# Kernel optimization log

Hardware: AMD Instinct MI355X
Metric: run time of the kernel (lower is better)

## Reference

```python
import jax, jax.numpy as jnp
import numpy as np

DIM = 512
HEADS = 8
DIM_HEAD = 64
HIDDEN = HEADS * DIM_HEAD  # 512
B, N, M = 4, 2048, 2048


def setup_inputs() -> dict:
    key = jax.random.key(0)
    ks = jax.random.split(key, 7)
    s = 0.02
    return {
        "x": jax.random.normal(ks[0], (B, N, DIM), jnp.float32),
        "context": jax.random.normal(ks[1], (B, M, DIM), jnp.float32),
        "Wq": jax.random.normal(ks[2], (DIM, HIDDEN), jnp.float32) * s,
        "Wk": jax.random.normal(ks[3], (DIM, HIDDEN), jnp.float32) * s,
        "Wv": jax.random.normal(ks[4], (DIM, HIDDEN), jnp.float32) * s,
        "Wo": jax.random.normal(ks[5], (HIDDEN, DIM), jnp.float32) * s,
        "bo": jnp.zeros((DIM,), jnp.float32),
    }


def reference(x, context, Wq, Wk, Wv, Wo, bo):
    scale = DIM_HEAD ** (-0.5)
    # projections: [B, N, HIDDEN] -> [B, H, N, D]
    def split_heads(t):
        b, n, _ = t.shape
        return t.reshape(b, n, HEADS, DIM_HEAD).transpose(0, 2, 1, 3)
    q = split_heads(x @ Wq)
    k = split_heads(context @ Wk)
    v = split_heads(context @ Wv)
    # scores: [B, H, N, M]
    sim = jnp.einsum('bhid,bhjd->bhij', q, k) * scale
    attn = jax.nn.softmax(sim, axis=-1)
    out = jnp.einsum('bhij,bhjd->bhid', attn, v)  # [B, H, N, D]
    out = out.transpose(0, 2, 1, 3).reshape(x.shape[0], x.shape[1], HIDDEN)
    return out @ Wo + bo
```

## Files before the change

### kernel.cpp

```cpp
#include <hip/hip_runtime.h>
#include <hip/hip_bf16.h>


typedef __attribute__((ext_vector_type(8))) short bf16x8;
typedef __attribute__((ext_vector_type(4))) float f32x4;

#define MFMA16(a, b, c) __builtin_amdgcn_mfma_f32_16x16x32_bf16(a, b, c, 0, 0, 0)
#define SCALE_LOG2E 0.18033688011112042f

static __device__ inline unsigned short f2b(float f) {
    __hip_bfloat16 h = __float2bfloat16(f);
    return __builtin_bit_cast(unsigned short, h);
}
static __device__ inline unsigned int pk_rnd(float hi, float lo) {
    unsigned uh = __builtin_bit_cast(unsigned, hi) + 0x8000u;
    unsigned ul = __builtin_bit_cast(unsigned, lo) + 0x8000u;
    return __builtin_amdgcn_perm(uh, ul, 0x07060302);
}
static __device__ inline float fexp2(float x) {
    float r;
    asm("v_exp_f32 %0, %1" : "=v"(r) : "v"(x));
    return r;
}
static __device__ inline void gll16(const void* g, void* l) {
    __builtin_amdgcn_global_load_lds(
        (const __attribute__((address_space(1))) void*)g,
        (__attribute__((address_space(3))) void*)l, 16, 0, 0);
}

__global__ __launch_bounds__(256) void prep_kernel(const float* __restrict__ x,
                                                   const float* __restrict__ ctx,
                                                   const float* __restrict__ Wq,
                                                   const float* __restrict__ Wk,
                                                   const float* __restrict__ Wv,
                                                   const float* __restrict__ Wo,
                                                   unsigned short* __restrict__ xb,
                                                   unsigned short* __restrict__ cb,
                                                   unsigned short* __restrict__ wt_base) {
    __shared__ float T[64][65];
    const int bid = blockIdx.x, tid = threadIdx.x;
    if (bid < 8192) {
        const float* src = (bid < 4096) ? x : ctx;
        unsigned short* dst = (bid < 4096) ? xb : cb;
        int i = (bid & 4095) * 256 + tid;
        const float4 v = reinterpret_cast<const float4*>(src)[i];
        uint2 o;
        o.x = pk_rnd(v.y, v.x);
        o.y = pk_rnd(v.w, v.z);
        reinterpret_cast<uint2*>(dst)[i] = o;
        return;
    }
    const int b = bid - 8192;
    const int which = b >> 6, t6 = b & 63;
    const float* W = (which == 0) ? Wq : (which == 1) ? Wk : (which == 2) ? Wv : Wo;
    unsigned short* Wt = wt_base + (size_t)which * 512 * 512;
    const int n0 = (t6 & 7) * 64, k0 = (t6 >> 3) * 64;
    const int rr = tid >> 4, cc = (tid & 15) * 4;
    #pragma unroll
    for (int i = 0; i < 4; i++) {
        const float4 v = *reinterpret_cast<const float4*>(&W[(size_t)(k0 + rr + 16 * i) * 512 + n0 + cc]);
        T[rr + 16 * i][cc + 0] = v.x; T[rr + 16 * i][cc + 1] = v.y;
        T[rr + 16 * i][cc + 2] = v.z; T[rr + 16 * i][cc + 3] = v.w;
    }
    __syncthreads();
    #pragma unroll
    for (int i = 0; i < 4; i++) {
        int n = rr + 16 * i;
        uint2 o;
        o.x = pk_rnd(T[cc + 1][n], T[cc + 0][n]);
        o.y = pk_rnd(T[cc + 3][n], T[cc + 2][n]);
        *reinterpret_cast<uint2*>(&Wt[(size_t)(n0 + n) * 512 + k0 + cc]) = o;
    }
}

__device__ inline void gemm_tile_128(const unsigned short* __restrict__ A,
                                     const unsigned short* __restrict__ Bt,
                                     int row0, int col0, f32x4 acc[4][4]) {
    __shared__ unsigned short As[128 * 32];
    __shared__ unsigned short Bs[128 * 32];
    const int tid  = threadIdx.x;
    const int lane = tid & 63, wave = tid >> 6;
    const int quad = lane >> 4, mr = lane & 15;
    const int m_off = (wave & 1) * 64, n_off = (wave >> 1) * 64;

    const int lrow = lane >> 2;
    const int lq   = (lane & 3) ^ (lrow & 3);
    const unsigned short* aSrc = A  + (size_t)(row0 + wave * 32 + lrow) * 512 + lq * 8;
    const unsigned short* bSrc = Bt + (size_t)(col0 + wave * 32 + lrow) * 512 + lq * 8;
    unsigned short* aL0 = &As[(wave * 32) * 32];
    unsigned short* aL1 = &As[(wave * 32 + 16) * 32];
    unsigned short* bL0 = &Bs[(wave * 32) * 32];
    unsigned short* bL1 = &Bs[(wave * 32 + 16) * 32];

    for (int kt = 0; kt < 16; kt++) {
        __syncthreads();
        gll16(aSrc + kt * 32, aL0);
        gll16(aSrc + 16 * 512 + kt * 32, aL1);
        gll16(bSrc + kt * 32, bL0);
        gll16(bSrc + 16 * 512 + kt * 32, bL1);
        __syncthreads();
        bf16x8 af[4], bfr[4];
        #pragma unroll
        for (int i = 0; i < 4; i++) {
            int m = m_off + i * 16 + mr;
            af[i] = *reinterpret_cast<const bf16x8*>(&As[m * 32 + ((quad ^ (m & 3)) * 8)]);
        }
        #pragma unroll
        for (int j = 0; j < 4; j++) {
            int n = n_off + j * 16 + mr;
            bfr[j] = *reinterpret_cast<const bf16x8*>(&Bs[n * 32 + ((quad ^ (n & 3)) * 8)]);
        }
        #pragma unroll
        for (int i = 0; i < 4; i++)
            #pragma unroll
            for (int j = 0; j < 4; j++)
                acc[i][j] = MFMA16(af[i], bfr[j], acc[i][j]);
    }
}

__global__ __launch_bounds__(256) void gemm_proj_kernel(const unsigned short* __restrict__ xb,
                                                        const unsigned short* __restrict__ cb,
                                                        const unsigned short* __restrict__ wt_base,
                                                        unsigned short* __restrict__ qkv_base) {
    const int f = blockIdx.x, g = f & 7, j = f >> 3;
    const int xt = j & 3;
    const int ry = g + 8 * ((j >> 2) & 7);
    const int which = j >> 5;

    const unsigned short* A  = (which == 0) ? xb : cb;
    const unsigned short* Bt = wt_base + (size_t)which * 512 * 512;
    unsigned short* out      = qkv_base + (size_t)which * 8192 * 512;

    f32x4 acc[4][4];
    #pragma unroll
    for (int i = 0; i < 4; i++)
        #pragma unroll
        for (int j2 = 0; j2 < 4; j2++) acc[i][j2] = (f32x4){0.f, 0.f, 0.f, 0.f};

    gemm_tile_128(A, Bt, ry * 128, xt * 128, acc);

    const int lane = threadIdx.x & 63, wave = threadIdx.x >> 6;
    const int quad = lane >> 4, mr = lane & 15;
    const int m_off = (wave & 1) * 64, n_off = (wave >> 1) * 64;
    const float qs = (which == 0) ? SCALE_LOG2E : 1.0f;

    if (which == 2) {
        #pragma unroll
        for (int i = 0; i < 4; i++) {
            #pragma unroll
            for (int j2 = 0; j2 < 4; j2++) {
                int gcol = xt * 128 + n_off + j2 * 16 + mr;
                int h = gcol >> 6, d = gcol & 63;
                int grow = ry * 128 + m_off + i * 16 + quad * 4;
                int b = grow >> 11, n = grow & 2047;
                uint2 o;
                o.x = pk_rnd(acc[i][j2][1], acc[i][j2][0]);
                o.y = pk_rnd(acc[i][j2][3], acc[i][j2][2]);
                *reinterpret_cast<uint2*>(&out[((size_t)(b * 8 + h) * 64 + d) * 2048 + n]) = o;
            }
        }
    } else {
        #pragma unroll
        for (int i = 0; i < 4; i++) {
            #pragma unroll
            for (int j2 = 0; j2 < 4; j2++) {
                int gcol = xt * 128 + n_off + j2 * 16 + mr;
                int h = gcol >> 6, d = gcol & 63;
                #pragma unroll
                for (int r = 0; r < 4; r++) {
                    int grow = ry * 128 + m_off + i * 16 + quad * 4 + r;
                    int b = grow >> 11, n = grow & 2047;
                    out[((size_t)(b * 8 + h) * 2048 + n) * 64 + d] = f2b(acc[i][j2][r] * qs);
                }
            }
        }
    }
}

__global__ __launch_bounds__(256) void flash_kernel(const unsigned short* __restrict__ qw,
                                                    const unsigned short* __restrict__ kw,
                                                    const unsigned short* __restrict__ vt,
                                                    float* __restrict__ p0,
                                                    float* __restrict__ p1,
                                                    float* __restrict__ l0,
                                                    float* __restrict__ l1) {
    __shared__ unsigned short Ks[64 * 72];
    __shared__ unsigned short Vs[64 * 72];
    __shared__ unsigned short Pw[4][32 * 72];

    const int f = blockIdx.x, g = f & 7, j = f >> 3;
    const int qtile = j & 15;
    const int kidx  = (j >> 4) & 1;
    const int bh    = g + 8 * (j >> 5);

    const int tid  = threadIdx.x;
    const int lane = tid & 63, wave = tid >> 6;
    const int quad = lane >> 4, mr = lane & 15;

    const unsigned short* qbase = qw + ((size_t)bh * 2048 + qtile * 128 + wave * 32) * 64;
    const unsigned short* kbase = kw + (size_t)bh * 2048 * 64;
    const unsigned short* vbase = vt + (size_t)bh * 64 * 2048;
    float* Pdst = kidx ? p1 : p0;
    float* ldst = kidx ? l1 : l0;

    bf16x8 qf[2][2];
    #pragma unroll
    for (int gq = 0; gq < 2; gq++) {
        qf[gq][0] = *reinterpret_cast<const bf16x8*>(qbase + (gq * 16 + mr) * 64 + quad * 8);
        qf[gq][1] = *reinterpret_cast<const bf16x8*>(qbase + (gq * 16 + mr) * 64 + 32 + quad * 8);
    }

    bf16x8 ones;
    #pragma unroll
    for (int e = 0; e < 8; e++) ones[e] = (short)0x3F80;

    f32x4 oacc[2][4], lacc[2];
    #pragma unroll
    for (int gq = 0; gq < 2; gq++) {
        lacc[gq] = (f32x4){0.f, 0.f, 0.f, 0.f};
        #pragma unroll
        for (int nt = 0; nt < 4; nt++) oacc[gq][nt] = (f32x4){0.f, 0.f, 0.f, 0.f};
    }

    const int srow = tid >> 2, soff = (tid & 3) * 16;

    const int kbeg = kidx * 1024;
    for (int key0 = kbeg; key0 < kbeg + 1024; key0 += 64) {
        __syncthreads();
        {
            const uint4* kp = reinterpret_cast<const uint4*>(kbase + (size_t)(key0 + srow) * 64 + soff);
            uint4* kd = reinterpret_cast<uint4*>(&Ks[srow * 72 + soff]);
            kd[0] = kp[0]; kd[1] = kp[1];
            const uint4* vp = reinterpret_cast<const uint4*>(vbase + (size_t)srow * 2048 + key0 + soff);
            uint4* vd = reinterpret_cast<uint4*>(&Vs[srow * 72 + soff]);
            vd[0] = vp[0]; vd[1] = vp[1];
        }
        __syncthreads();

        f32x4 sv[2][4];
        #pragma unroll
        for (int gq = 0; gq < 2; gq++)
            #pragma unroll
            for (int kt = 0; kt < 4; kt++) sv[gq][kt] = (f32x4){0.f, 0.f, 0.f, 0.f};
        #pragma unroll
        for (int c = 0; c < 2; c++) {
            #pragma unroll
            for (int kt = 0; kt < 4; kt++) {
                bf16x8 kf = *reinterpret_cast<const bf16x8*>(&Ks[(kt * 16 + mr) * 72 + c * 32 + quad * 8]);
                sv[0][kt] = MFMA16(kf, qf[0][c], sv[0][kt]);
                sv[1][kt] = MFMA16(kf, qf[1][c], sv[1][kt]);
            }
        }

        #pragma unroll
        for (int gq = 0; gq < 2; gq++) {
            #pragma unroll
            for (int kt = 0; kt < 4; kt++) {
                uint2 w;
                w.x = pk_rnd(fexp2(sv[gq][kt][1]), fexp2(sv[gq][kt][0]));
                w.y = pk_rnd(fexp2(sv[gq][kt][3]), fexp2(sv[gq][kt][2]));
                *reinterpret_cast<uint2*>(&Pw[wave][(gq * 16 + mr) * 72 + kt * 16 + quad * 4]) = w;
            }
        }
        asm volatile("s_waitcnt lgkmcnt(0)" ::: "memory");

        #pragma unroll
        for (int ks = 0; ks < 2; ks++) {
            bf16x8 pf0 = *reinterpret_cast<const bf16x8*>(&Pw[wave][(mr) * 72 + ks * 32 + quad * 8]);
            bf16x8 pf1 = *reinterpret_cast<const bf16x8*>(&Pw[wave][(16 + mr) * 72 + ks * 32 + quad * 8]);
            lacc[0] = MFMA16(pf0, ones, lacc[0]);
            lacc[1] = MFMA16(pf1, ones, lacc[1]);
            #pragma unroll
            for (int nt = 0; nt < 4; nt++) {
                bf16x8 vf = *reinterpret_cast<const bf16x8*>(&Vs[(nt * 16 + mr) * 72 + ks * 32 + quad * 8]);
                oacc[0][nt] = MFMA16(pf0, vf, oacc[0][nt]);
                oacc[1][nt] = MFMA16(pf1, vf, oacc[1][nt]);
            }
        }
    }

    const int b = bh >> 3, h = bh & 7;
    #pragma unroll
    for (int gq = 0; gq < 2; gq++) {
        #pragma unroll
        for (int nt = 0; nt < 4; nt++) {
            #pragma unroll
            for (int r = 0; r < 4; r++) {
                int row = qtile * 128 + wave * 32 + gq * 16 + quad * 4 + r;
                Pdst[((size_t)b * 2048 + row) * 512 + h * 64 + nt * 16 + mr] = oacc[gq][nt][r];
            }
        }
        if (mr == 0) {
            #pragma unroll
            for (int r = 0; r < 4; r++) {
                int row = qtile * 128 + wave * 32 + gq * 16 + quad * 4 + r;
                ldst[(size_t)bh * 2048 + row] = lacc[gq][r];
            }
        }
    }
}

__global__ __launch_bounds__(256) void combine_kernel(const float* __restrict__ p0,
                                                      const float* __restrict__ p1,
                                                      const float* __restrict__ l0,
                                                      const float* __restrict__ l1,
                                                      unsigned short* __restrict__ ob) {
    const int idx = blockIdx.x * 256 + threadIdx.x;
    const size_t flat = (size_t)idx * 4;
    const int row = (int)(flat >> 9);
    const int c   = (int)(flat & 511);
    const int bh  = (row >> 11) * 8 + (c >> 6);
    const int qn  = row & 2047;
    const float lv = l0[(size_t)bh * 2048 + qn] + l1[(size_t)bh * 2048 + qn];
    const float li = 1.0f / lv;
    const float4 a = reinterpret_cast<const float4*>(p0)[idx];
    const float4 bb = reinterpret_cast<const float4*>(p1)[idx];
    uint2 o;
    o.x = pk_rnd((a.y + bb.y) * li, (a.x + bb.x) * li);
    o.y = pk_rnd((a.w + bb.w) * li, (a.z + bb.z) * li);
    reinterpret_cast<uint2*>(ob)[idx] = o;
}

__global__ __launch_bounds__(256) void gemm_out_kernel(const unsigned short* __restrict__ obuf,
                                                       const unsigned short* __restrict__ Wot,
                                                       const float* __restrict__ bo,
                                                       float* __restrict__ out) {
    const int f = blockIdx.x, g = f & 7, j = f >> 3;
    const int xt = j & 3;
    const int ry = g + 8 * (j >> 2);

    f32x4 acc[4][4];
    #pragma unroll
    for (int i = 0; i < 4; i++)
        #pragma unroll
        for (int j2 = 0; j2 < 4; j2++) acc[i][j2] = (f32x4){0.f, 0.f, 0.f, 0.f};

    gemm_tile_128(obuf, Wot, ry * 128, xt * 128, acc);

    const int lane = threadIdx.x & 63, wave = threadIdx.x >> 6;
    const int quad = lane >> 4, mr = lane & 15;
    const int m_off = (wave & 1) * 64, n_off = (wave >> 1) * 64;
    #pragma unroll
    for (int i = 0; i < 4; i++) {
        #pragma unroll
        for (int j2 = 0; j2 < 4; j2++) {
            int gcol = xt * 128 + n_off + j2 * 16 + mr;
            float bias = bo[gcol];
            #pragma unroll
            for (int r = 0; r < 4; r++) {
                int grow = ry * 128 + m_off + i * 16 + quad * 4 + r;
                out[(size_t)grow * 512 + gcol] = acc[i][j2][r] + bias;
            }
        }
    }
}

extern "C" void kernel_launch(void* const* d_in, const int* in_sizes, int n_in,
                              void* d_out, int out_size, void* d_ws, size_t ws_size,
                              hipStream_t stream) {
    const float* x   = (const float*)d_in[0];
    const float* ctx = (const float*)d_in[1];
    const float* Wq  = (const float*)d_in[2];
    const float* Wk  = (const float*)d_in[3];
    const float* Wv  = (const float*)d_in[4];
    const float* Wo  = (const float*)d_in[5];
    const float* bo  = (const float*)d_in[6];
    float* out = (float*)d_out;

    unsigned short* ws  = (unsigned short*)d_ws;
    unsigned short* xb  = ws;
    unsigned short* cb  = xb + (size_t)8192 * 512;
    unsigned short* Wt  = cb + (size_t)8192 * 512;
    unsigned short* qkv = Wt + (size_t)4 * 512 * 512;
    unsigned short* ob  = qkv + (size_t)3 * 8192 * 512;

    float* p0 = out;
    float* p1 = (float*)xb;
    float* l0 = (float*)Wt;
    float* l1 = (float*)(Wt + (size_t)512 * 512);

    prep_kernel<<<8448, 256, 0, stream>>>(x, ctx, Wq, Wk, Wv, Wo, xb, cb, Wt);
    gemm_proj_kernel<<<768, 256, 0, stream>>>(xb, cb, Wt, qkv);
    flash_kernel<<<1024, 256, 0, stream>>>(qkv, qkv + (size_t)8192 * 512,
                                           qkv + (size_t)2 * 8192 * 512, p0, p1, l0, l1);
    combine_kernel<<<4096, 256, 0, stream>>>(p0, p1, l0, l1, ob);
    gemm_out_kernel<<<256, 256, 0, stream>>>(ob, Wt + (size_t)3 * 512 * 512, bo, out);
}
```

Measured before the change: 188.6 us.

## Fuse fp32-to-bf16 conversion into projection GEMM and combine into output GEMM

The separate activation-conversion pass is removed. The projection GEMM now loads fp32 x/context directly, rounds it to bf16 in registers and writes the result to LDS. The combine kernel is also folded into the output GEMM's A-tile load, which sums the two flash partials and scales by 1/l before packing to bf16. This drops two memory-bound kernels and their intermediate buffers, at the cost of synchronous register loads in the GEMM main loop and redundant reads of the fp32 A tiles across the column-tile blocks.

```diff
diff --git a/kernel.cpp b/kernel.cpp
--- a/kernel.cpp
+++ b/kernel.cpp
@@ -28,29 +28,13 @@
         (__attribute__((address_space(3))) void*)l, 16, 0, 0);
 }
 
-__global__ __launch_bounds__(256) void prep_kernel(const float* __restrict__ x,
-                                                   const float* __restrict__ ctx,
-                                                   const float* __restrict__ Wq,
-                                                   const float* __restrict__ Wk,
-                                                   const float* __restrict__ Wv,
-                                                   const float* __restrict__ Wo,
-                                                   unsigned short* __restrict__ xb,
-                                                   unsigned short* __restrict__ cb,
-                                                   unsigned short* __restrict__ wt_base) {
+__global__ __launch_bounds__(256) void transw_kernel(const float* __restrict__ Wq,
+                                                     const float* __restrict__ Wk,
+                                                     const float* __restrict__ Wv,
+                                                     const float* __restrict__ Wo,
+                                                     unsigned short* __restrict__ wt_base) {
     __shared__ float T[64][65];
-    const int bid = blockIdx.x, tid = threadIdx.x;
-    if (bid < 8192) {
-        const float* src = (bid < 4096) ? x : ctx;
-        unsigned short* dst = (bid < 4096) ? xb : cb;
-        int i = (bid & 4095) * 256 + tid;
-        const float4 v = reinterpret_cast<const float4*>(src)[i];
-        uint2 o;
-        o.x = pk_rnd(v.y, v.x);
-        o.y = pk_rnd(v.w, v.z);
-        reinterpret_cast<uint2*>(dst)[i] = o;
-        return;
-    }
-    const int b = bid - 8192;
+    const int b = blockIdx.x, tid = threadIdx.x;
     const int which = b >> 6, t6 = b & 63;
     const float* W = (which == 0) ? Wq : (which == 1) ? Wk : (which == 2) ? Wv : Wo;
     unsigned short* Wt = wt_base + (size_t)which * 512 * 512;
@@ -73,77 +57,82 @@
     }
 }
 
-__device__ inline void gemm_tile_128(const unsigned short* __restrict__ A,
-                                     const unsigned short* __restrict__ Bt,
-                                     int row0, int col0, f32x4 acc[4][4]) {
+__device__ inline void gemm_frags_mfma(const unsigned short* As, const unsigned short* Bs,
+                                       int m_off, int n_off, int quad, int mr,
+                                       f32x4 acc[4][4]) {
+    bf16x8 af[4], bfr[4];
+    #pragma unroll
+    for (int i = 0; i < 4; i++) {
+        int m = m_off + i * 16 + mr;
+        af[i] = *reinterpret_cast<const bf16x8*>(&As[m * 32 + ((quad ^ (m & 3)) * 8)]);
+    }
+    #pragma unroll
+    for (int j = 0; j < 4; j++) {
+        int n = n_off + j * 16 + mr;
+        bfr[j] = *reinterpret_cast<const bf16x8*>(&Bs[n * 32 + ((quad ^ (n & 3)) * 8)]);
+    }
+    #pragma unroll
+    for (int i = 0; i < 4; i++)
+        #pragma unroll
+        for (int j = 0; j < 4; j++)
+            acc[i][j] = MFMA16(af[i], bfr[j], acc[i][j]);
+}
+
+__global__ __launch_bounds__(256) void gemm_proj_kernel(const float* __restrict__ x,
+                                                        const float* __restrict__ ctx,
+                                                        const unsigned short* __restrict__ wt_base,
+                                                        unsigned short* __restrict__ qkv_base) {
     __shared__ unsigned short As[128 * 32];
     __shared__ unsigned short Bs[128 * 32];
+    const int f = blockIdx.x, g = f & 7, j = f >> 3;
+    const int xt = j & 3;
+    const int ry = g + 8 * ((j >> 2) & 7);
+    const int which = j >> 5;
+
+    const float* A32         = (which == 0) ? x : ctx;
+    const unsigned short* Bt = wt_base + (size_t)which * 512 * 512;
+    unsigned short* out      = qkv_base + (size_t)which * 8192 * 512;
+
     const int tid  = threadIdx.x;
     const int lane = tid & 63, wave = tid >> 6;
     const int quad = lane >> 4, mr = lane & 15;
     const int m_off = (wave & 1) * 64, n_off = (wave >> 1) * 64;
-
     const int lrow = lane >> 2;
     const int lq   = (lane & 3) ^ (lrow & 3);
-    const unsigned short* aSrc = A  + (size_t)(row0 + wave * 32 + lrow) * 512 + lq * 8;
-    const unsigned short* bSrc = Bt + (size_t)(col0 + wave * 32 + lrow) * 512 + lq * 8;
-    unsigned short* aL0 = &As[(wave * 32) * 32];
-    unsigned short* aL1 = &As[(wave * 32 + 16) * 32];
+
+    const float* aF0 = A32 + (size_t)(ry * 128 + wave * 32 + lrow) * 512 + lq * 8;
+    const float* aF1 = aF0 + 16 * 512;
+    const unsigned short* bSrc = Bt + (size_t)(xt * 128 + wave * 32 + lrow) * 512 + lq * 8;
     unsigned short* bL0 = &Bs[(wave * 32) * 32];
     unsigned short* bL1 = &Bs[(wave * 32 + 16) * 32];
+    uint4* aW0 = reinterpret_cast<uint4*>(&As[(wave * 32 + lrow) * 32 + (lane & 3) * 8]);
+    uint4* aW1 = reinterpret_cast<uint4*>(&As[(wave * 32 + 16 + lrow) * 32 + (lane & 3) * 8]);
+
+    f32x4 acc[4][4];
+    #pragma unroll
+    for (int i = 0; i < 4; i++)
+        #pragma unroll
+        for (int j2 = 0; j2 < 4; j2++) acc[i][j2] = (f32x4){0.f, 0.f, 0.f, 0.f};
 
     for (int kt = 0; kt < 16; kt++) {
-        __syncthreads();
-        gll16(aSrc + kt * 32, aL0);
-        gll16(aSrc + 16 * 512 + kt * 32, aL1);
+        const float4 f0 = *reinterpret_cast<const float4*>(aF0 + kt * 32);
+        const float4 f1 = *reinterpret_cast<const float4*>(aF0 + kt * 32 + 4);
+        const float4 f2 = *reinterpret_cast<const float4*>(aF1 + kt * 32);
+        const float4 f3 = *reinterpret_cast<const float4*>(aF1 + kt * 32 + 4);
+        __syncthreads();
         gll16(bSrc + kt * 32, bL0);
         gll16(bSrc + 16 * 512 + kt * 32, bL1);
-        __syncthreads();
-        bf16x8 af[4], bfr[4];
-        #pragma unroll
-        for (int i = 0; i < 4; i++) {
-            int m = m_off + i * 16 + mr;
-            af[i] = *reinterpret_cast<const bf16x8*>(&As[m * 32 + ((quad ^ (m & 3)) * 8)]);
-        }
-        #pragma unroll
-        for (int j = 0; j < 4; j++) {
-            int n = n_off + j * 16 + mr;
-            bfr[j] = *reinterpret_cast<const bf16x8*>(&Bs[n * 32 + ((quad ^ (n & 3)) * 8)]);
-        }
-        #pragma unroll
-        for (int i = 0; i < 4; i++)
-            #pragma unroll
-            for (int j = 0; j < 4; j++)
-                acc[i][j] = MFMA16(af[i], bfr[j], acc[i][j]);
-    }
-}
-
-__global__ __launch_bounds__(256) void gemm_proj_kernel(const unsigned short* __restrict__ xb,
-                                                        const unsigned short* __restrict__ cb,
-                                                        const unsigned short* __restrict__ wt_base,
-                                                        unsigned short* __restrict__ qkv_base) {
-    const int f = blockIdx.x, g = f & 7, j = f >> 3;
-    const int xt = j & 3;
-    const int ry = g + 8 * ((j >> 2) & 7);
-    const int which = j >> 5;
-
-    const unsigned short* A  = (which == 0) ? xb : cb;
-    const unsigned short* Bt = wt_base + (size_t)which * 512 * 512;
-    unsigned short* out      = qkv_base + (size_t)which * 8192 * 512;
-
-    f32x4 acc[4][4];
-    #pragma unroll
-    for (int i = 0; i < 4; i++)
-        #pragma unroll
-        for (int j2 = 0; j2 < 4; j2++) acc[i][j2] = (f32x4){0.f, 0.f, 0.f, 0.f};
-
-    gemm_tile_128(A, Bt, ry * 128, xt * 128, acc);
-
-    const int lane = threadIdx.x & 63, wave = threadIdx.x >> 6;
-    const int quad = lane >> 4, mr = lane & 15;
-    const int m_off = (wave & 1) * 64, n_off = (wave >> 1) * 64;
+        uint4 u0, u1;
+        u0.x = pk_rnd(f0.y, f0.x); u0.y = pk_rnd(f0.w, f0.z);
+        u0.z = pk_rnd(f1.y, f1.x); u0.w = pk_rnd(f1.w, f1.z);
+        u1.x = pk_rnd(f2.y, f2.x); u1.y = pk_rnd(f2.w, f2.z);
+        u1.z = pk_rnd(f3.y, f3.x); u1.w = pk_rnd(f3.w, f3.z);
+        *aW0 = u0; *aW1 = u1;
+        __syncthreads();
+        gemm_frags_mfma(As, Bs, m_off, n_off, quad, mr, acc);
+    }
+
     const float qs = (which == 0) ? SCALE_LOG2E : 1.0f;
-
     if (which == 2) {
         #pragma unroll
         for (int i = 0; i < 4; i++) {
@@ -300,46 +289,82 @@
     }
 }
 
-__global__ __launch_bounds__(256) void combine_kernel(const float* __restrict__ p0,
-                                                      const float* __restrict__ p1,
-                                                      const float* __restrict__ l0,
-                                                      const float* __restrict__ l1,
-                                                      unsigned short* __restrict__ ob) {
-    const int idx = blockIdx.x * 256 + threadIdx.x;
-    const size_t flat = (size_t)idx * 4;
-    const int row = (int)(flat >> 9);
-    const int c   = (int)(flat & 511);
-    const int bh  = (row >> 11) * 8 + (c >> 6);
-    const int qn  = row & 2047;
-    const float lv = l0[(size_t)bh * 2048 + qn] + l1[(size_t)bh * 2048 + qn];
-    const float li = 1.0f / lv;
-    const float4 a = reinterpret_cast<const float4*>(p0)[idx];
-    const float4 bb = reinterpret_cast<const float4*>(p1)[idx];
-    uint2 o;
-    o.x = pk_rnd((a.y + bb.y) * li, (a.x + bb.x) * li);
-    o.y = pk_rnd((a.w + bb.w) * li, (a.z + bb.z) * li);
-    reinterpret_cast<uint2*>(ob)[idx] = o;
-}
-
-__global__ __launch_bounds__(256) void gemm_out_kernel(const unsigned short* __restrict__ obuf,
+__global__ __launch_bounds__(256) void gemm_out_kernel(const float* __restrict__ p0,
+                                                       const float* __restrict__ p1,
+                                                       const float* __restrict__ l0,
+                                                       const float* __restrict__ l1,
                                                        const unsigned short* __restrict__ Wot,
                                                        const float* __restrict__ bo,
                                                        float* __restrict__ out) {
+    __shared__ unsigned short As[128 * 32];
+    __shared__ unsigned short Bs[128 * 32];
     const int f = blockIdx.x, g = f & 7, j = f >> 3;
     const int xt = j & 3;
     const int ry = g + 8 * (j >> 2);
 
-    f32x4 acc[4][4];
-    #pragma unroll
-    for (int i = 0; i < 4; i++)
-        #pragma unroll
-        for (int j2 = 0; j2 < 4; j2++) acc[i][j2] = (f32x4){0.f, 0.f, 0.f, 0.f};
-
-    gemm_tile_128(obuf, Wot, ry * 128, xt * 128, acc);
-
-    const int lane = threadIdx.x & 63, wave = threadIdx.x >> 6;
+    const int tid  = threadIdx.x;
+    const int lane = tid & 63, wave = tid >> 6;
     const int quad = lane >> 4, mr = lane & 15;
     const int m_off = (wave & 1) * 64, n_off = (wave >> 1) * 64;
+    const int lrow = lane >> 2;
+    const int lq   = (lane & 3) ^ (lrow & 3);
+
+    const int grA = ry * 128 + wave * 32 + lrow;
+    const int grB = grA + 16;
+    const int bb  = grA >> 11;
+    const int qnA = grA & 2047, qnB = grB & 2047;
+
+    float liA[8], liB[8];
+    #pragma unroll
+    for (int h = 0; h < 8; h++) {
+        size_t ia = (size_t)(bb * 8 + h) * 2048;
+        liA[h] = 1.0f / (l0[ia + qnA] + l1[ia + qnA]);
+        liB[h] = 1.0f / (l0[ia + qnB] + l1[ia + qnB]);
+    }
+
+    const float* q0a = p0 + (size_t)grA * 512 + lq * 8;
+    const float* q0b = p0 + (size_t)grB * 512 + lq * 8;
+    const float* q1a = p1 + (size_t)grA * 512 + lq * 8;
+    const float* q1b = p1 + (size_t)grB * 512 + lq * 8;
+    const unsigned short* bSrc = Wot + (size_t)(xt * 128 + wave * 32 + lrow) * 512 + lq * 8;
+    unsigned short* bL0 = &Bs[(wave * 32) * 32];
+    unsigned short* bL1 = &Bs[(wave * 32 + 16) * 32];
+    uint4* aW0 = reinterpret_cast<uint4*>(&As[(wave * 32 + lrow) * 32 + (lane & 3) * 8]);
+    uint4* aW1 = reinterpret_cast<uint4*>(&As[(wave * 32 + 16 + lrow) * 32 + (lane & 3) * 8]);
+
+    f32x4 acc[4][4];
+    #pragma unroll
+    for (int i = 0; i < 4; i++)
+        #pragma unroll
+        for (int j2 = 0; j2 < 4; j2++) acc[i][j2] = (f32x4){0.f, 0.f, 0.f, 0.f};
+
+    for (int kt = 0; kt < 16; kt++) {
+        const float4 x0 = *reinterpret_cast<const float4*>(q0a + kt * 32);
+        const float4 x1 = *reinterpret_cast<const float4*>(q0a + kt * 32 + 4);
+        const float4 y0 = *reinterpret_cast<const float4*>(q1a + kt * 32);
+        const float4 y1 = *reinterpret_cast<const float4*>(q1a + kt * 32 + 4);
+        const float4 x2 = *reinterpret_cast<const float4*>(q0b + kt * 32);
+        const float4 x3 = *reinterpret_cast<const float4*>(q0b + kt * 32 + 4);
+        const float4 y2 = *reinterpret_cast<const float4*>(q1b + kt * 32);
+        const float4 y3 = *reinterpret_cast<const float4*>(q1b + kt * 32 + 4);
+        __syncthreads();
+        gll16(bSrc + kt * 32, bL0);
+        gll16(bSrc + 16 * 512 + kt * 32, bL1);
+        const float sA = liA[kt >> 1], sB = liB[kt >> 1];
+        uint4 u0, u1;
+        u0.x = pk_rnd((x0.y + y0.y) * sA, (x0.x + y0.x) * sA);
+        u0.y = pk_rnd((x0.w + y0.w) * sA, (x0.z + y0.z) * sA);
+        u0.z = pk_rnd((x1.y + y1.y) * sA, (x1.x + y1.x) * sA);
+        u0.w = pk_rnd((x1.w + y1.w) * sA, (x1.z + y1.z) * sA);
+        u1.x = pk_rnd((x2.y + y2.y) * sB, (x2.x + y2.x) * sB);
+        u1.y = pk_rnd((x2.w + y2.w) * sB, (x2.z + y2.z) * sB);
+        u1.z = pk_rnd((x3.y + y3.y) * sB, (x3.x + y3.x) * sB);
+        u1.w = pk_rnd((x3.w + y3.w) * sB, (x3.z + y3.z) * sB);
+        *aW0 = u0; *aW1 = u1;
+        __syncthreads();
+        gemm_frags_mfma(As, Bs, m_off, n_off, quad, mr, acc);
+    }
+
     #pragma unroll
     for (int i = 0; i < 4; i++) {
         #pragma unroll
@@ -368,21 +393,17 @@
     float* out = (float*)d_out;
 
     unsigned short* ws  = (unsigned short*)d_ws;
-    unsigned short* xb  = ws;
-    unsigned short* cb  = xb + (size_t)8192 * 512;
-    unsigned short* Wt  = cb + (size_t)8192 * 512;
+    unsigned short* Wt  = ws;
     unsigned short* qkv = Wt + (size_t)4 * 512 * 512;
-    unsigned short* ob  = qkv + (size_t)3 * 8192 * 512;
-
-    float* p0 = out;
-    float* p1 = (float*)xb;
+    float* p0 = (float*)(qkv + (size_t)3 * 8192 * 512);
+    float* p1 = p0 + (size_t)8192 * 512;
     float* l0 = (float*)Wt;
     float* l1 = (float*)(Wt + (size_t)512 * 512);
 
-    prep_kernel<<<8448, 256, 0, stream>>>(x, ctx, Wq, Wk, Wv, Wo, xb, cb, Wt);
-    gemm_proj_kernel<<<768, 256, 0, stream>>>(xb, cb, Wt, qkv);
+    transw_kernel<<<256, 256, 0, stream>>>(Wq, Wk, Wv, Wo, Wt);
+    gemm_proj_kernel<<<768, 256, 0, stream>>>(x, ctx, Wt, qkv);
     flash_kernel<<<1024, 256, 0, stream>>>(qkv, qkv + (size_t)8192 * 512,
                                            qkv + (size_t)2 * 8192 * 512, p0, p1, l0, l1);
-    combine_kernel<<<4096, 256, 0, stream>>>(p0, p1, l0, l1, ob);
-    gemm_out_kernel<<<256, 256, 0, stream>>>(ob, Wt + (size_t)3 * 512 * 512, bo, out);
-}
+    gemm_out_kernel<<<256, 256, 0, stream>>>(p0, p1, l0, l1,
+                                             Wt + (size_t)3 * 512 * 512, bo, out);
+}
```

After: 191.1 us. About the same (+1.3%).
